# Optimization experiments

Measured on AMD Instinct MI355X. Metric: run time of the kernel, lower is better.

Reference implementation:

```python
import jax, jax.numpy as jnp
import numpy as np

B, Tin, Tout = 256, 32, 29
Venc, Vdec = 29, 72
E = 256; H = 256; L = 3; G = 4 * H; D = 2 * L  # bidirectional dirs * layers


def lstm_step(x, h, c, Wih0, Wih1, Whh, b):
    """One timestep of a 3-layer bidirectional LSTM (torch gate order i,f,g,o).
    x: [B, in], h/c: [D, B, H] in torch layout (layer-major, dir-minor)."""
    new_h, new_c = [], []
    inp = x
    for l in range(L):
        outs = []
        for d in range(2):
            idx = 2 * l + d
            Wih = Wih0[d] if l == 0 else Wih1[l - 1, d]
            g = inp @ Wih.T + h[idx] @ Whh[l, d].T + b[l, d]
            i_g, f_g, g_g, o_g = jnp.split(g, 4, axis=-1)
            cc = jax.nn.sigmoid(f_g) * c[idx] + jax.nn.sigmoid(i_g) * jnp.tanh(g_g)
            hh = jax.nn.sigmoid(o_g) * jnp.tanh(cc)
            new_h.append(hh); new_c.append(cc); outs.append(hh)
        inp = jnp.concatenate(outs, axis=-1)  # feeds next layer: [B, 2H]
    return jnp.stack(new_h), jnp.stack(new_c), inp


def proj(hid, W1, b1, W2, b2):
    """Linear over hidden dim then Linear over the layer*dir dim -- the exact
    math of torch's linear1 -> permute(2,1,0) -> linear2 -> permute(2,1,0)."""
    hn = jnp.einsum('lbh,gh->lbg', hid, W1) + b1            # [D, B, H]
    return jnp.einsum('lbh,ml->mbh', hn, W2) + b2[:, None, None]


def setup_inputs() -> dict:
    key = jax.random.key(0)
    ks = iter(jax.random.split(key, 64))
    def p(shape, scale=0.06):
        return jax.random.normal(next(ks), shape, jnp.float32) * scale
    return {
        "input": jax.random.randint(next(ks), (B, Tin), 0, Venc),
        "target": jax.random.randint(next(ks), (B, Tout), 0, Vdec),
        "teacher_force": 1,
        "enc_emb": p((Venc, E)), "dec_emb": p((Vdec, E)),
        "enc_Wih0": p((2, G, E)), "enc_Wih1": p((L - 1, 2, G, 2 * H)),
        "enc_Whh": p((L, 2, G, H)), "enc_b": p((L, 2, G)),
        "dec_Wih0": p((2, G, E)), "dec_Wih1": p((L - 1, 2, G, 2 * H)),
        "dec_Whh": p((L, 2, G, H)), "dec_b": p((L, 2, G)),
        "lin_h_W1": p((H, H)), "lin_h_b1": p((H,)), "lin_h_W2": p((D, D)), "lin_h_b2": p((D,)),
        "lin_c_W1": p((H, H)), "lin_c_b1": p((H,)), "lin_c_W2": p((D, D)), "lin_c_b2": p((D,)),
        "lin_a_W1": p((H, H)), "lin_a_b1": p((H,)), "lin_a_W2": p((D, D)), "lin_a_b2": p((D,)),
        "attn_W": p((E, E + H)), "attn_b": p((E,)),
        "fc_W": p((Vdec, 2 * H)), "fc_b": p((Vdec,)),
    }


def reference(input, target, teacher_force, enc_emb, dec_emb, enc_Wih0, enc_Wih1, enc_Whh, enc_b, dec_Wih0, dec_Wih1, dec_Whh, dec_b, lin_h_W1, lin_h_b1, lin_h_W2, lin_h_b2, lin_c_W1, lin_c_b1, lin_c_W2, lin_c_b2, lin_a_W1, lin_a_b1, lin_a_W2, lin_a_b2, attn_W, attn_b, fc_W, fc_b):
    Bb = input.shape[0]
    h0 = jnp.zeros((D, Bb, H), jnp.float32)

    # ---- encoder: step LSTM over Tin, projecting hidden per step for attention ----
    def enc_step(carry, x_t):
        h, c = carry
        h, c, _ = lstm_step(enc_emb[x_t], h, c, enc_Wih0, enc_Wih1, enc_Whh, enc_b)
        return (h, c), proj(h, lin_a_W1, lin_a_b1, lin_a_W2, lin_a_b2)

    (h, c), encoder_outputs = jax.lax.scan(enc_step, (h0, h0), input.T)  # [Tin, D, B, H]

    # ---- encoder->decoder state bridging (linear over H, linear over D) ----
    dec_h = proj(h, lin_h_W1, lin_h_b1, lin_h_W2, lin_h_b2)
    dec_c = proj(c, lin_c_W1, lin_c_b1, lin_c_W2, lin_c_b2)

    def dec_core(h, c, tok):
        emb = dec_emb[tok]                                # [B, E]
        energies = h[None] * encoder_outputs              # [Tin, D, B, H]
        aw = jax.nn.softmax(energies, axis=0)             # attn over source time
        ctx = (aw * encoder_outputs).sum(0).mean(0)       # [B, H]
        x = jnp.concatenate([emb, ctx], -1) @ attn_W.T + attn_b
        h, c, top = lstm_step(x, h, c, dec_Wih0, dec_Wih1, dec_Whh, dec_b)
        return h, c, top @ fc_W.T + fc_b, aw.sum(-1)      # logits [B,V], aw [Tin,D,B]

    if teacher_force:
        def step(carry, tok):
            h, c = carry
            h, c, logits, _ = dec_core(h, c, tok)
            return (h, c), logits
        _, logits_seq = jax.lax.scan(step, (dec_h, dec_c), target[:, :Tout - 1].T)
        attn_seq = jnp.zeros((Tout - 1, Tin, D, Bb), jnp.float32)
    else:
        def step(carry, _):
            h, c, tok = carry
            h, c, logits, aw = dec_core(h, c, tok)
            nxt = jnp.argmax(jax.nn.softmax(logits, -1), -1).astype(tok.dtype)
            return (h, c, nxt), (logits, aw)
        tok0 = jnp.ones((Bb,), input.dtype)
        _, (logits_seq, attn_seq) = jax.lax.scan(step, (dec_h, dec_c, tok0), None, length=Tout - 1)

    pred0 = jnp.zeros((1, Bb, Vdec), jnp.float32).at[0, :, 1].set(1.0)
    predicted = jnp.concatenate([pred0, logits_seq], 0)   # [Tout, B, Vdec]
    attn_weights = jnp.concatenate([jnp.zeros((1, Tin, D, Bb), jnp.float32), attn_seq], 0)
    return predicted, attn_weights
```

## Files before the change

kernel.cpp:

```cpp
#include <hip/hip_runtime.h>
#include <math.h>

#define BB 256
#define TIN 32
#define TOUT 29
#define VDEC 72
#define EDIM 256
#define HDIM 256
#define DD 6
#define BH (BB*HDIM)

typedef unsigned short u16;
typedef unsigned int u32;
typedef __bf16 bf16x8 __attribute__((ext_vector_type(8)));
typedef float f32x4 __attribute__((ext_vector_type(4)));
typedef u16 u16x8 __attribute__((ext_vector_type(8)));

__device__ __forceinline__ float sigmf(float x){ return 1.0f/(1.0f+expf(-x)); }
__device__ __forceinline__ u16 f2bf(float f){
  u32 u = __builtin_bit_cast(u32, f);
  u32 r = (u + 0x7fffu + ((u>>16)&1u)) >> 16;
  return (u16)r;
}
__device__ __forceinline__ float bf2f(u16 s){
  u32 u = ((u32)s)<<16; return __builtin_bit_cast(float, u);
}
__device__ __forceinline__ bf16x8 ldbf8(const u16* p){
  u16x8 t = *(const u16x8*)p; return __builtin_bit_cast(bf16x8, t);
}
__device__ __forceinline__ f32x4 mfma16(bf16x8 a, bf16x8 b, f32x4 c){
  return __builtin_amdgcn_mfma_f32_16x16x32_bf16(a, b, c, 0, 0, 0);
}

__global__ void fill_zero_u32(u32* __restrict__ p, int n){
  int i = blockIdx.x*256 + threadIdx.x;
  if (i < n) p[i] = 0u;
}

__global__ void init_out_kernel(float* __restrict__ out, int n){
  int i = blockIdx.x*256 + threadIdx.x;
  if (i >= n) return;
  float v = 0.0f;
  if (i < BB*VDEC && (i % VDEC) == 1) v = 1.0f;
  out[i] = v;
}

__global__ void bias2d_kernel(const float* __restrict__ W2a, const float* __restrict__ b1a, const float* __restrict__ b2a,
                              const float* __restrict__ W2h, const float* __restrict__ b1h, const float* __restrict__ b2h,
                              const float* __restrict__ W2c, const float* __restrict__ b1c, const float* __restrict__ b2c,
                              float* __restrict__ outp){
  int g = threadIdx.x;
  const float* W2[3] = {W2a, W2h, W2c};
  const float* b1[3] = {b1a, b1h, b1c};
  const float* b2[3] = {b2a, b2h, b2c};
  for (int p = 0; p < 3; p++)
    for (int m = 0; m < 6; m++){
      float s = 0.f;
      for (int l = 0; l < 6; l++) s += W2[p][m*6+l];
      outp[p*1536 + m*256 + g] = s * b1[p][g] + b2[p][m];
    }
}

__global__ void embed_enc_kernel(const int* __restrict__ input, const float* __restrict__ enc_emb,
                                 u16* __restrict__ x_emb){
  int i = blockIdx.x*256 + threadIdx.x;
  int e = i & 255, b = (i >> 8) & 255, t = i >> 16;
  x_emb[i] = f2bf(enc_emb[(size_t)input[b*TIN + t]*EDIM + e]);
}

__global__ void pack_w_kernel(const float* __restrict__ Wih, const float* __restrict__ Whh,
                              u16* __restrict__ dst, int K1, int K, int permute){
  int k = blockIdx.x*256 + threadIdx.x;
  int row = blockIdx.y;
  int d = row >> 10, rr = row & 1023;
  int g;
  if (permute){
    int ht = rr >> 6, r = rr & 63;
    g = (r>>4)*256 + ht*16 + (r&15);
  } else g = rr;
  float v;
  if (k < K1) v = Wih[((size_t)d*1024 + g)*K1 + k];
  else        v = Whh[((size_t)d*1024 + g)*256 + (k - K1)];
  dst[(size_t)row*K + k] = f2bf(v);
}

__global__ void mix_kernel(const float* __restrict__ inp, float* __restrict__ outp,
                           const float* __restrict__ W2, int n){
  int i = blockIdx.x*256 + threadIdx.x;
  if (i >= n) return;
  int h = i & 255, b = (i >> 8) & 255, t = i >> 16;
  size_t base = ((size_t)t*6)*BH + (size_t)b*256 + h;
  float v[6];
  #pragma unroll
  for (int l = 0; l < 6; l++) v[l] = inp[base + (size_t)l*BH];
  #pragma unroll
  for (int m = 0; m < 6; m++){
    float s = 0.f;
    #pragma unroll
    for (int l = 0; l < 6; l++) s += W2[m*6+l]*v[l];
    outp[base + (size_t)m*BH] = s;
  }
}

__global__ __launch_bounds__(256) void gemmN256_kernel(const float* __restrict__ A, float* __restrict__ C,
                                                       const float* __restrict__ W,
                                                       const float* __restrict__ bias2d,
                                                       u16* __restrict__ Cbf){
  __shared__ float As[32][33];
  __shared__ float Ws[256][34];
  int tid = threadIdx.x;
  int m_base = blockIdx.x * 32;
  int rg = tid >> 5, cg = tid & 31;
  float acc[4][8];
  #pragma unroll
  for (int i=0;i<4;i++)
    #pragma unroll
    for (int j=0;j<8;j++) acc[i][j]=0.f;
  for (int k0 = 0; k0 < 256; k0 += 32){
    #pragma unroll
    for (int p=0;p<4;p++) As[rg + p*8][cg] = A[(size_t)(m_base + rg + p*8)*256 + k0 + cg];
    #pragma unroll
    for (int p=0;p<32;p++) Ws[rg + p*8][cg] = W[(size_t)(rg + p*8)*256 + k0 + cg];
    __syncthreads();
    #pragma unroll
    for (int kk=0; kk<32; kk++){
      float a[4], w[8];
      #pragma unroll
      for (int i=0;i<4;i++) a[i] = As[rg*4+i][kk];
      #pragma unroll
      for (int j=0;j<8;j++) w[j] = Ws[cg*8+j][kk];
      #pragma unroll
      for (int i=0;i<4;i++)
        #pragma unroll
        for (int j=0;j<8;j++) acc[i][j] += a[i]*w[j];
    }
    __syncthreads();
  }
  #pragma unroll
  for (int i=0;i<4;i++){
    int row = m_base + rg*4 + i;
    int bm = (row >> 8) % 6;
    #pragma unroll
    for (int j=0;j<8;j++){
      float v = acc[i][j] + bias2d[bm*256 + cg*8 + j];
      C[(size_t)row*256 + cg*8 + j] = v;
      if (Cbf) Cbf[(size_t)row*256 + cg*8 + j] = f2bf(v);
    }
  }
}

__global__ __launch_bounds__(256) void lstm_stage_mfma(
    const u16* __restrict__ inp, int lda, int K1,
    const u16* __restrict__ Wpk,
    const float* __restrict__ bias_l,
    const u16* __restrict__ hR, u16* __restrict__ hW,
    float* __restrict__ cBuf, u16* __restrict__ inp_out,
    float* __restrict__ h_all_t, int l){
  __shared__ __align__(16) u16 As[32][72];
  __shared__ __align__(16) u16 Ws[64][72];
  __shared__ float Gt[4][32][17];
  int tid = threadIdx.x;
  int m_base = blockIdx.x*32;
  int d = blockIdx.y >> 4, ht = blockIdx.y & 15;
  int idx = 2*l + d;
  int K = K1 + 256;
  const u16* Wblk = Wpk + (size_t)((d*16+ht)*64)*K;
  const u16* A2 = hR + (size_t)idx*BH;
  int q = tid >> 6, lane = tid & 63;
  int ar = tid >> 3, kp = (tid & 7)*8;
  f32x4 acc0 = {0.f,0.f,0.f,0.f}, acc1 = {0.f,0.f,0.f,0.f};
  for (int c0 = 0; c0 < K; c0 += 64){
    int col = c0 + kp;
    const u16* ap = (col < K1) ? inp + (size_t)(m_base+ar)*lda + col
                               : A2  + (size_t)(m_base+ar)*HDIM + (col - K1);
    uint4 av  = *(const uint4*)ap;
    uint4 wv0 = *(const uint4*)(Wblk + (size_t)ar*K + col);
    uint4 wv1 = *(const uint4*)(Wblk + (size_t)(ar+32)*K + col);
    __syncthreads();
    *(uint4*)&As[ar][kp] = av;
    *(uint4*)&Ws[ar][kp] = wv0;
    *(uint4*)&Ws[ar+32][kp] = wv1;
    __syncthreads();
    #pragma unroll
    for (int kh = 0; kh < 2; kh++){
      int kb = kh*32 + (lane>>4)*8;
      bf16x8 a0 = ldbf8(&As[lane & 15][kb]);
      bf16x8 a1 = ldbf8(&As[16 + (lane & 15)][kb]);
      bf16x8 bq = ldbf8(&Ws[q*16 + (lane & 15)][kb]);
      acc0 = mfma16(a0, bq, acc0);
      acc1 = mfma16(a1, bq, acc1);
    }
  }
  int hh = lane & 15, rq = lane >> 4;
  #pragma unroll
  for (int r = 0; r < 4; r++){
    Gt[q][rq*4 + r][hh]      = acc0[r];
    Gt[q][16 + rq*4 + r][hh] = acc1[r];
  }
  __syncthreads();
  const float* bias = bias_l + d*1024;
  #pragma unroll
  for (int it = 0; it < 2; it++){
    int id = tid + it*256;
    int bb = id >> 4, h2 = id & 15;
    int b = m_base + bb, h = ht*16 + h2;
    float iv = Gt[0][bb][h2] + bias[h];
    float fv = Gt[1][bb][h2] + bias[256 + h];
    float gv = Gt[2][bb][h2] + bias[512 + h];
    float ov = Gt[3][bb][h2] + bias[768 + h];
    size_t off = (size_t)idx*BH + (size_t)b*HDIM + h;
    float cold = cBuf[off];
    float cc = sigmf(fv)*cold + sigmf(iv)*tanhf(gv);
    float hv = sigmf(ov)*tanhf(cc);
    cBuf[off] = cc;
    u16 hb = f2bf(hv);
    hW[off] = hb;
    inp_out[(size_t)b*512 + d*HDIM + h] = hb;
    if (h_all_t) h_all_t[off] = hv;
  }
}

__global__ __launch_bounds__(256) void xw_mfma(
    const u16* __restrict__ emb, const u16* __restrict__ ctx,
    const u16* __restrict__ Wpk, const float* __restrict__ bias,
    u16* __restrict__ xw){
  __shared__ __align__(16) u16 As[32][72];
  __shared__ __align__(16) u16 Ws[64][72];
  int tid = threadIdx.x;
  int m_base = blockIdx.x*32;
  int n_base = blockIdx.y*64;
  int q = tid >> 6, lane = tid & 63;
  int ar = tid >> 3, kp = (tid & 7)*8;
  const u16* Wblk = Wpk + (size_t)n_base*512;
  f32x4 acc0 = {0.f,0.f,0.f,0.f}, acc1 = {0.f,0.f,0.f,0.f};
  for (int c0 = 0; c0 < 512; c0 += 64){
    int col = c0 + kp;
    const u16* ap = (col < 256) ? emb + (size_t)(m_base+ar)*256 + col
                                : ctx + (size_t)(m_base+ar)*256 + (col - 256);
    uint4 av  = *(const uint4*)ap;
    uint4 wv0 = *(const uint4*)(Wblk + (size_t)ar*512 + col);
    uint4 wv1 = *(const uint4*)(Wblk + (size_t)(ar+32)*512 + col);
    __syncthreads();
    *(uint4*)&As[ar][kp] = av;
    *(uint4*)&Ws[ar][kp] = wv0;
    *(uint4*)&Ws[ar+32][kp] = wv1;
    __syncthreads();
    #pragma unroll
    for (int kh = 0; kh < 2; kh++){
      int kb = kh*32 + (lane>>4)*8;
      bf16x8 a0 = ldbf8(&As[lane & 15][kb]);
      bf16x8 a1 = ldbf8(&As[16 + (lane & 15)][kb]);
      bf16x8 bq = ldbf8(&Ws[q*16 + (lane & 15)][kb]);
      acc0 = mfma16(a0, bq, acc0);
      acc1 = mfma16(a1, bq, acc1);
    }
  }
  int hh = lane & 15, rq = lane >> 4;
  int n = n_base + q*16 + hh;
  float bv = bias[n];
  #pragma unroll
  for (int r = 0; r < 4; r++){
    xw[(size_t)(m_base + rq*4 + r)*256 + n]      = f2bf(acc0[r] + bv);
    xw[(size_t)(m_base + 16 + rq*4 + r)*256 + n] = f2bf(acc1[r] + bv);
  }
}

__global__ void attn_tok_kernel(const u16* __restrict__ hR, const float* __restrict__ eo,
                                u16* __restrict__ ctx, const int* __restrict__ tf,
                                float* __restrict__ attn_out, int step,
                                const int* __restrict__ target, const float* __restrict__ pred,
                                const float* __restrict__ dec_emb, u16* __restrict__ emb){
  int blk = blockIdx.x, tid = threadIdx.x;
  if (blk < 256){
    int i = blk*256 + tid;
    int hc = i & 255, b = i >> 8;
    bool wa = (tf[0] == 0);
    float acc = 0.f;
    for (int d = 0; d < DD; d++){
      float hv = bf2f(hR[(size_t)d*BH + (size_t)b*256 + hc]);
      const float* ep = eo + (size_t)d*BH + (size_t)b*256 + hc;
      float se = 0.f, ac = 0.f;
      for (int t = 0; t < TIN; t++){
        float ev = ep[(size_t)t*(DD*BH)];
        float e = expf(hv*ev);
        se += e; ac += e*ev;
      }
      acc += ac/se;
      if (wa){
        float inv = 1.f/se;
        for (int t = 0; t < TIN; t++){
          float ev = ep[(size_t)t*(DD*BH)];
          atomicAdd(&attn_out[(((size_t)(step+1)*TIN + t)*DD + d)*BB + b], expf(hv*ev)*inv);
        }
      }
    }
    ctx[i] = f2bf(acc*(1.0f/6.0f));
  } else {
    int j = (blk - 256)*256 + tid;
    int b = j >> 6, e4 = (j & 63)*4;
    int tok;
    if (tf[0]) tok = target[b*TOUT + step];
    else if (step == 0) tok = 1;
    else {
      const float* lg = pred + ((size_t)step*BB + b)*VDEC;
      tok = 0; float bv = lg[0];
      for (int v = 1; v < VDEC; v++){ float x = lg[v]; if (x > bv){ bv = x; tok = v; } }
    }
    #pragma unroll
    for (int r = 0; r < 4; r++)
      emb[(size_t)b*EDIM + e4 + r] = f2bf(dec_emb[(size_t)tok*EDIM + e4 + r]);
  }
}

__global__ void fc_kernel(const u16* __restrict__ top, const float* __restrict__ fc_W,
                          const float* __restrict__ fc_b, float* __restrict__ outp, int step){
  __shared__ float s[512];
  int b = blockIdx.x, tid = threadIdx.x;
  s[tid]       = bf2f(top[(size_t)b*512 + tid]);
  s[tid + 256] = bf2f(top[(size_t)b*512 + 256 + tid]);
  __syncthreads();
  if (tid < VDEC){
    float a = fc_b[tid];
    for (int k = 0; k < 512; k++) a += s[k]*fc_W[(size_t)tid*512 + k];
    outp[((size_t)(step+1)*BB + b)*VDEC + tid] = a;
  }
}


extern "C" void kernel_launch(void* const* d_in, const int* in_sizes, int n_in,
                              void* d_out, int out_size, void* d_ws, size_t ws_size,
                              hipStream_t stream){
  (void)in_sizes; (void)n_in; (void)out_size; (void)ws_size;
  const int*   input    = (const int*)d_in[0];
  const int*   target   = (const int*)d_in[1];
  const int*   tf       = (const int*)d_in[2];
  const float* enc_emb  = (const float*)d_in[3];
  const float* dec_emb  = (const float*)d_in[4];
  const float* enc_Wih0 = (const float*)d_in[5];
  const float* enc_Wih1 = (const float*)d_in[6];
  const float* enc_Whh  = (const float*)d_in[7];
  const float* enc_b    = (const float*)d_in[8];
  const float* dec_Wih0 = (const float*)d_in[9];
  const float* dec_Wih1 = (const float*)d_in[10];
  const float* dec_Whh  = (const float*)d_in[11];
  const float* dec_b    = (const float*)d_in[12];
  const float* lin_h_W1 = (const float*)d_in[13];
  const float* lin_h_b1 = (const float*)d_in[14];
  const float* lin_h_W2 = (const float*)d_in[15];
  const float* lin_h_b2 = (const float*)d_in[16];
  const float* lin_c_W1 = (const float*)d_in[17];
  const float* lin_c_b1 = (const float*)d_in[18];
  const float* lin_c_W2 = (const float*)d_in[19];
  const float* lin_c_b2 = (const float*)d_in[20];
  const float* lin_a_W1 = (const float*)d_in[21];
  const float* lin_a_b1 = (const float*)d_in[22];
  const float* lin_a_W2 = (const float*)d_in[23];
  const float* lin_a_b2 = (const float*)d_in[24];
  const float* attn_W   = (const float*)d_in[25];
  const float* attn_b   = (const float*)d_in[26];
  const float* fc_W     = (const float*)d_in[27];
  const float* fc_b     = (const float*)d_in[28];
  float* out = (float*)d_out;

  char* base = (char*)d_ws;
  size_t off = 0;
  auto alloc = [&](size_t bytes)->char*{
    char* p = base + off; off += (bytes + 255) & ~(size_t)255; return p;
  };
  float* h_all  = (float*)alloc(sizeof(float)*(size_t)TIN*DD*BH);
  float* tmp6   = (float*)alloc(sizeof(float)*(size_t)DD*BH);
  float* dec_c  = (float*)alloc(sizeof(float)*(size_t)DD*BH);
  float* bias2d = (float*)alloc(sizeof(float)*3*6*256);
  u16*   enc_hA = (u16*)alloc(sizeof(u16)*(size_t)DD*BH + sizeof(float)*(size_t)DD*BH);
  float* enc_c  = (float*)(enc_hA + (size_t)DD*BH);
  u16* enc_hB = (u16*)alloc(sizeof(u16)*(size_t)DD*BH);
  u16* dec_hA = (u16*)alloc(sizeof(u16)*(size_t)DD*BH);
  u16* dec_hB = (u16*)alloc(sizeof(u16)*(size_t)DD*BH);
  u16* x_emb  = (u16*)alloc(sizeof(u16)*(size_t)TIN*BB*EDIM);
  u16* bufA   = (u16*)alloc(sizeof(u16)*(size_t)BB*512);
  u16* bufB   = (u16*)alloc(sizeof(u16)*(size_t)BB*512);
  u16* emb    = (u16*)alloc(sizeof(u16)*(size_t)BB*256);
  u16* ctxb   = (u16*)alloc(sizeof(u16)*(size_t)BB*256);
  u16* xw     = (u16*)alloc(sizeof(u16)*(size_t)BB*256);
  u16* wp_e0  = (u16*)alloc(sizeof(u16)*(size_t)2048*512);
  u16* wp_e1  = (u16*)alloc(sizeof(u16)*(size_t)2048*768);
  u16* wp_e2  = (u16*)alloc(sizeof(u16)*(size_t)2048*768);
  u16* wp_d0  = (u16*)alloc(sizeof(u16)*(size_t)2048*512);
  u16* wp_d1  = (u16*)alloc(sizeof(u16)*(size_t)2048*768);
  u16* wp_d2  = (u16*)alloc(sizeof(u16)*(size_t)2048*768);
  u16* wp_at  = (u16*)alloc(sizeof(u16)*(size_t)256*512);

  const int outn = TOUT*BB*VDEC + TOUT*TIN*DD*BB;
  init_out_kernel<<<(outn+255)/256, 256, 0, stream>>>(out, outn);
  fill_zero_u32<<<(DD*BH*6/4 + 255)/256, 256, 0, stream>>>((u32*)enc_hA, DD*BH*6/4);
  bias2d_kernel<<<1, 256, 0, stream>>>(lin_a_W2, lin_a_b1, lin_a_b2,
                                       lin_h_W2, lin_h_b1, lin_h_b2,
                                       lin_c_W2, lin_c_b1, lin_c_b2, bias2d);
  embed_enc_kernel<<<(TIN*BB*EDIM)/256, 256, 0, stream>>>(input, enc_emb, x_emb);
  pack_w_kernel<<<dim3(2,2048), 256, 0, stream>>>(enc_Wih0, enc_Whh,                       wp_e0, 256, 512, 1);
  pack_w_kernel<<<dim3(3,2048), 256, 0, stream>>>(enc_Wih1, enc_Whh + 2*1024*256,          wp_e1, 512, 768, 1);
  pack_w_kernel<<<dim3(3,2048), 256, 0, stream>>>(enc_Wih1 + (size_t)2*1024*512, enc_Whh + 4*1024*256, wp_e2, 512, 768, 1);
  pack_w_kernel<<<dim3(2,2048), 256, 0, stream>>>(dec_Wih0, dec_Whh,                       wp_d0, 256, 512, 1);
  pack_w_kernel<<<dim3(3,2048), 256, 0, stream>>>(dec_Wih1, dec_Whh + 2*1024*256,          wp_d1, 512, 768, 1);
  pack_w_kernel<<<dim3(3,2048), 256, 0, stream>>>(dec_Wih1 + (size_t)2*1024*512, dec_Whh + 4*1024*256, wp_d2, 512, 768, 1);
  pack_w_kernel<<<dim3(2,256),  256, 0, stream>>>(attn_W, attn_W ,               wp_at, 512, 512, 0);

  dim3 sgrid(8, 32);
  for (int t = 0; t < TIN; t++){
    const u16* hRb = (t & 1) ? enc_hB : enc_hA;
    u16*       hWb = (t & 1) ? enc_hA : enc_hB;
    float* hat = h_all + (size_t)t*DD*BH;
    lstm_stage_mfma<<<sgrid,256,0,stream>>>(x_emb + (size_t)t*BB*EDIM, 256, 256, wp_e0,
        enc_b,        hRb, hWb, enc_c, bufA, hat, 0);
    lstm_stage_mfma<<<sgrid,256,0,stream>>>(bufA, 512, 512, wp_e1,
        enc_b + 2048, hRb, hWb, enc_c, bufB, hat, 1);
    lstm_stage_mfma<<<sgrid,256,0,stream>>>(bufB, 512, 512, wp_e2,
        enc_b + 4096, hRb, hWb, enc_c, bufA, hat, 2);
  }
  mix_kernel<<<BH/256, 256, 0, stream>>>(h_all + (size_t)31*DD*BH, tmp6, lin_h_W2, BH);
  gemmN256_kernel<<<(DD*BB)/32, 256, 0, stream>>>(tmp6, tmp6, lin_h_W1, bias2d + 1536, dec_hA);
  mix_kernel<<<BH/256, 256, 0, stream>>>(enc_c, tmp6, lin_c_W2, BH);
  gemmN256_kernel<<<(DD*BB)/32, 256, 0, stream>>>(tmp6, dec_c, lin_c_W1, bias2d + 3072, nullptr);
  mix_kernel<<<(TIN*BH)/256, 256, 0, stream>>>(h_all, h_all, lin_a_W2, TIN*BH);
  gemmN256_kernel<<<(TIN*DD*BB)/32, 256, 0, stream>>>(h_all, h_all, lin_a_W1, bias2d, nullptr);

  float* attn_out = out + (size_t)TOUT*BB*VDEC;
  for (int i = 0; i < TOUT-1; i++){
    const u16* hRb = (i & 1) ? dec_hB : dec_hA;
    u16*       hWb = (i & 1) ? dec_hA : dec_hB;
    attn_tok_kernel<<<320, 256, 0, stream>>>(hRb, h_all, ctxb, tf, attn_out, i,
                                             target, out, dec_emb, emb);
    xw_mfma<<<dim3(8,4), 256, 0, stream>>>(emb, ctxb, wp_at, attn_b, xw);
    lstm_stage_mfma<<<sgrid,256,0,stream>>>(xw, 256, 256, wp_d0,
        dec_b,        hRb, hWb, dec_c, bufA, nullptr, 0);
    lstm_stage_mfma<<<sgrid,256,0,stream>>>(bufA, 512, 512, wp_d1,
        dec_b + 2048, hRb, hWb, dec_c, bufB, nullptr, 1);
    lstm_stage_mfma<<<sgrid,256,0,stream>>>(bufB, 512, 512, wp_d2,
        dec_b + 4096, hRb, hWb, dec_c, bufA, nullptr, 2);
    fc_kernel<<<BB, 256, 0, stream>>>(bufA, fc_W, fc_b, out, i);
  }
}
```

Measured before the change: 3.463 ms.

## Fuse encoder/decoder loops into one persistent kernel with grid barriers

Replaces roughly two hundred per-step kernel launches with a single persistent mega-kernel of 256 blocks that synchronise through an atomic-counter grid barrier. It also folds the attention projection into the first decoder layer's weights, stores encoder outputs in bf16 with a batch-major layout, and moves the projection GEMMs to MFMA. The aim is to remove launch overhead and inter-kernel gaps on the serial recurrence. The trade-offs are that the spin barrier assumes all 256 blocks are co-resident, and bf16 storage of the attention keys adds rounding error.

```diff
diff --git a/kernel.cpp b/kernel.cpp
--- a/kernel.cpp
+++ b/kernel.cpp
@@ -9,6 +9,7 @@
 #define HDIM 256
 #define DD 6
 #define BH (BB*HDIM)
+#define NB 256
 
 typedef unsigned short u16;
 typedef unsigned int u32;
@@ -31,6 +32,7 @@
 __device__ __forceinline__ f32x4 mfma16(bf16x8 a, bf16x8 b, f32x4 c){
   return __builtin_amdgcn_mfma_f32_16x16x32_bf16(a, b, c, 0, 0, 0);
 }
+
 
 __global__ void fill_zero_u32(u32* __restrict__ p, int n){
   int i = blockIdx.x*256 + threadIdx.x;
@@ -69,102 +71,96 @@
 }
 
 __global__ void pack_w_kernel(const float* __restrict__ Wih, const float* __restrict__ Whh,
-                              u16* __restrict__ dst, int K1, int K, int permute){
+                              u16* __restrict__ dst, int K1, int K){
   int k = blockIdx.x*256 + threadIdx.x;
   int row = blockIdx.y;
   int d = row >> 10, rr = row & 1023;
-  int g;
-  if (permute){
-    int ht = rr >> 6, r = rr & 63;
-    g = (r>>4)*256 + ht*16 + (r&15);
-  } else g = rr;
+  int g = ((rr>>4)&3)*256 + (rr>>6)*16 + (rr&15);
   float v;
   if (k < K1) v = Wih[((size_t)d*1024 + g)*K1 + k];
   else        v = Whh[((size_t)d*1024 + g)*256 + (k - K1)];
   dst[(size_t)row*K + k] = f2bf(v);
 }
 
-__global__ void mix_kernel(const float* __restrict__ inp, float* __restrict__ outp,
-                           const float* __restrict__ W2, int n){
+__global__ void pack3_kernel(const float* __restrict__ a, const float* __restrict__ b, const float* __restrict__ c,
+                             u16* __restrict__ oa, u16* __restrict__ ob, u16* __restrict__ oc){
   int i = blockIdx.x*256 + threadIdx.x;
-  if (i >= n) return;
-  int h = i & 255, b = (i >> 8) & 255, t = i >> 16;
-  size_t base = ((size_t)t*6)*BH + (size_t)b*256 + h;
-  float v[6];
+  oa[i] = f2bf(a[i]); ob[i] = f2bf(b[i]); oc[i] = f2bf(c[i]);
+}
+
+__global__ __launch_bounds__(256) void comp_w_kernel(
+    const float* __restrict__ Wih0, const float* __restrict__ Whh0,
+    const float* __restrict__ attn_W, const float* __restrict__ attn_b,
+    const float* __restrict__ dec_b0, u16* __restrict__ wpk, float* __restrict__ b0p){
+  __shared__ float sw[8][256];
+  __shared__ float red[256];
+  int tid = threadIdx.x;
+  int rbase = blockIdx.x*8;
+  int gs[8], ds[8];
+  for (int r = 0; r < 8; r++){
+    int row = rbase + r;
+    int d = row >> 10, rr = row & 1023;
+    int g = ((rr>>4)&3)*256 + (rr>>6)*16 + (rr&15);
+    gs[r] = g; ds[r] = d;
+    sw[r][tid] = Wih0[((size_t)d*1024 + g)*256 + tid];
+  }
+  __syncthreads();
+  float a0[8], a1[8];
   #pragma unroll
-  for (int l = 0; l < 6; l++) v[l] = inp[base + (size_t)l*BH];
-  #pragma unroll
-  for (int m = 0; m < 6; m++){
-    float s = 0.f;
-    #pragma unroll
-    for (int l = 0; l < 6; l++) s += W2[m*6+l]*v[l];
-    outp[base + (size_t)m*BH] = s;
-  }
-}
-
-__global__ __launch_bounds__(256) void gemmN256_kernel(const float* __restrict__ A, float* __restrict__ C,
-                                                       const float* __restrict__ W,
-                                                       const float* __restrict__ bias2d,
-                                                       u16* __restrict__ Cbf){
-  __shared__ float As[32][33];
-  __shared__ float Ws[256][34];
-  int tid = threadIdx.x;
-  int m_base = blockIdx.x * 32;
-  int rg = tid >> 5, cg = tid & 31;
-  float acc[4][8];
-  #pragma unroll
-  for (int i=0;i<4;i++)
-    #pragma unroll
-    for (int j=0;j<8;j++) acc[i][j]=0.f;
-  for (int k0 = 0; k0 < 256; k0 += 32){
-    #pragma unroll
-    for (int p=0;p<4;p++) As[rg + p*8][cg] = A[(size_t)(m_base + rg + p*8)*256 + k0 + cg];
-    #pragma unroll
-    for (int p=0;p<32;p++) Ws[rg + p*8][cg] = W[(size_t)(rg + p*8)*256 + k0 + cg];
-    __syncthreads();
-    #pragma unroll
-    for (int kk=0; kk<32; kk++){
-      float a[4], w[8];
-      #pragma unroll
-      for (int i=0;i<4;i++) a[i] = As[rg*4+i][kk];
-      #pragma unroll
-      for (int j=0;j<8;j++) w[j] = Ws[cg*8+j][kk];
-      #pragma unroll
-      for (int i=0;i<4;i++)
-        #pragma unroll
-        for (int j=0;j<8;j++) acc[i][j] += a[i]*w[j];
-    }
-    __syncthreads();
-  }
-  #pragma unroll
-  for (int i=0;i<4;i++){
-    int row = m_base + rg*4 + i;
-    int bm = (row >> 8) % 6;
-    #pragma unroll
-    for (int j=0;j<8;j++){
-      float v = acc[i][j] + bias2d[bm*256 + cg*8 + j];
-      C[(size_t)row*256 + cg*8 + j] = v;
-      if (Cbf) Cbf[(size_t)row*256 + cg*8 + j] = f2bf(v);
-    }
-  }
-}
-
-__global__ __launch_bounds__(256) void lstm_stage_mfma(
+  for (int r = 0; r < 8; r++){ a0[r]=0.f; a1[r]=0.f; }
+  for (int e = 0; e < 256; e++){
+    float w0 = attn_W[(size_t)e*512 + tid];
+    float w1 = attn_W[(size_t)e*512 + 256 + tid];
+    #pragma unroll
+    for (int r = 0; r < 8; r++){ float s = sw[r][e]; a0[r] += s*w0; a1[r] += s*w1; }
+  }
+  for (int r = 0; r < 8; r++){
+    int row = rbase + r;
+    wpk[(size_t)row*768 + tid]       = f2bf(a0[r]);
+    wpk[(size_t)row*768 + 256 + tid] = f2bf(a1[r]);
+    wpk[(size_t)row*768 + 512 + tid] = f2bf(Whh0[((size_t)ds[r]*1024 + gs[r])*256 + tid]);
+  }
+  for (int r = 0; r < 8; r++){
+    red[tid] = sw[r][tid]*attn_b[tid];
+    __syncthreads();
+    for (int s2 = 128; s2 > 0; s2 >>= 1){ if (tid < s2) red[tid] += red[tid+s2]; __syncthreads(); }
+    if (tid == 0) b0p[ds[r]*1024 + gs[r]] = dec_b0[(size_t)ds[r]*1024 + gs[r]] + red[0];
+    __syncthreads();
+  }
+}
+
+
+__device__ __forceinline__ void gbar(int* cnt, int& ep){
+  __syncthreads();
+  ep++;
+  if (threadIdx.x == 0){
+    __threadfence();
+    __hip_atomic_fetch_add(cnt, 1, __ATOMIC_RELEASE, __HIP_MEMORY_SCOPE_AGENT);
+    int target = NB * ep;
+    while (__hip_atomic_load(cnt, __ATOMIC_ACQUIRE, __HIP_MEMORY_SCOPE_AGENT) < target)
+      __builtin_amdgcn_s_sleep(2);
+    __threadfence();
+  }
+  __syncthreads();
+}
+
+__device__ __forceinline__ void stage_unit(
     const u16* __restrict__ inp, int lda, int K1,
-    const u16* __restrict__ Wpk,
-    const float* __restrict__ bias_l,
+    const u16* __restrict__ Wpk, const float* __restrict__ bias_l,
     const u16* __restrict__ hR, u16* __restrict__ hW,
     float* __restrict__ cBuf, u16* __restrict__ inp_out,
-    float* __restrict__ h_all_t, int l){
-  __shared__ __align__(16) u16 As[32][72];
-  __shared__ __align__(16) u16 Ws[64][72];
-  __shared__ float Gt[4][32][17];
+    u16* __restrict__ h_all_t, int l, char* smem){
+  u16 (*As)[72] = (u16(*)[72])smem;
+  u16 (*Ws)[72] = (u16(*)[72])(smem + 4608);
+  float (*Gt)[32][17] = (float(*)[32][17])(smem + 13824);
   int tid = threadIdx.x;
-  int m_base = blockIdx.x*32;
-  int d = blockIdx.y >> 4, ht = blockIdx.y & 15;
+  int bid = blockIdx.x;
+  int m_base = (bid >> 5)*32;
+  int dht = bid & 31;
+  int d = dht >> 4, ht = dht & 15;
   int idx = 2*l + d;
   int K = K1 + 256;
-  const u16* Wblk = Wpk + (size_t)((d*16+ht)*64)*K;
+  const u16* Wblk = Wpk + (size_t)(dht*64)*K;
   const u16* A2 = hR + (size_t)idx*BH;
   int q = tid >> 6, lane = tid & 63;
   int ar = tid >> 3, kp = (tid & 7)*8;
@@ -184,11 +180,11 @@
     #pragma unroll
     for (int kh = 0; kh < 2; kh++){
       int kb = kh*32 + (lane>>4)*8;
-      bf16x8 a0 = ldbf8(&As[lane & 15][kb]);
-      bf16x8 a1 = ldbf8(&As[16 + (lane & 15)][kb]);
-      bf16x8 bq = ldbf8(&Ws[q*16 + (lane & 15)][kb]);
-      acc0 = mfma16(a0, bq, acc0);
-      acc1 = mfma16(a1, bq, acc1);
+      bf16x8 a0v = ldbf8(&As[lane & 15][kb]);
+      bf16x8 a1v = ldbf8(&As[16 + (lane & 15)][kb]);
+      bf16x8 bq  = ldbf8(&Ws[q*16 + (lane & 15)][kb]);
+      acc0 = mfma16(a0v, bq, acc0);
+      acc1 = mfma16(a1v, bq, acc1);
     }
   }
   int hh = lane & 15, rq = lane >> 4;
@@ -216,30 +212,25 @@
     u16 hb = f2bf(hv);
     hW[off] = hb;
     inp_out[(size_t)b*512 + d*HDIM + h] = hb;
-    if (h_all_t) h_all_t[off] = hv;
-  }
-}
-
-__global__ __launch_bounds__(256) void xw_mfma(
-    const u16* __restrict__ emb, const u16* __restrict__ ctx,
-    const u16* __restrict__ Wpk, const float* __restrict__ bias,
-    u16* __restrict__ xw){
-  __shared__ __align__(16) u16 As[32][72];
-  __shared__ __align__(16) u16 Ws[64][72];
+    if (h_all_t) h_all_t[off] = hb;
+  }
+}
+
+__device__ __forceinline__ void gemm_unit(
+    const u16* __restrict__ A, const u16* __restrict__ W,
+    const float* __restrict__ bias2, int r0, int n0, int mode,
+    u16* __restrict__ outb, float* __restrict__ outf, char* smem){
+  u16 (*As)[72] = (u16(*)[72])smem;
+  u16 (*Ws)[72] = (u16(*)[72])(smem + 4608);
   int tid = threadIdx.x;
-  int m_base = blockIdx.x*32;
-  int n_base = blockIdx.y*64;
   int q = tid >> 6, lane = tid & 63;
   int ar = tid >> 3, kp = (tid & 7)*8;
-  const u16* Wblk = Wpk + (size_t)n_base*512;
   f32x4 acc0 = {0.f,0.f,0.f,0.f}, acc1 = {0.f,0.f,0.f,0.f};
-  for (int c0 = 0; c0 < 512; c0 += 64){
+  for (int c0 = 0; c0 < 256; c0 += 64){
     int col = c0 + kp;
-    const u16* ap = (col < 256) ? emb + (size_t)(m_base+ar)*256 + col
-                                : ctx + (size_t)(m_base+ar)*256 + (col - 256);
-    uint4 av  = *(const uint4*)ap;
-    uint4 wv0 = *(const uint4*)(Wblk + (size_t)ar*512 + col);
-    uint4 wv1 = *(const uint4*)(Wblk + (size_t)(ar+32)*512 + col);
+    uint4 av  = *(const uint4*)(A + (size_t)(r0+ar)*256 + col);
+    uint4 wv0 = *(const uint4*)(W + (size_t)(n0+ar)*256 + col);
+    uint4 wv1 = *(const uint4*)(W + (size_t)(n0+ar+32)*256 + col);
     __syncthreads();
     *(uint4*)&As[ar][kp] = av;
     *(uint4*)&Ws[ar][kp] = wv0;
@@ -248,82 +239,202 @@
     #pragma unroll
     for (int kh = 0; kh < 2; kh++){
       int kb = kh*32 + (lane>>4)*8;
-      bf16x8 a0 = ldbf8(&As[lane & 15][kb]);
-      bf16x8 a1 = ldbf8(&As[16 + (lane & 15)][kb]);
-      bf16x8 bq = ldbf8(&Ws[q*16 + (lane & 15)][kb]);
-      acc0 = mfma16(a0, bq, acc0);
-      acc1 = mfma16(a1, bq, acc1);
+      bf16x8 a0v = ldbf8(&As[lane & 15][kb]);
+      bf16x8 a1v = ldbf8(&As[16 + (lane & 15)][kb]);
+      bf16x8 bq  = ldbf8(&Ws[q*16 + (lane & 15)][kb]);
+      acc0 = mfma16(a0v, bq, acc0);
+      acc1 = mfma16(a1v, bq, acc1);
     }
   }
   int hh = lane & 15, rq = lane >> 4;
-  int n = n_base + q*16 + hh;
-  float bv = bias[n];
+  int n = n0 + q*16 + hh;
   #pragma unroll
   for (int r = 0; r < 4; r++){
-    xw[(size_t)(m_base + rq*4 + r)*256 + n]      = f2bf(acc0[r] + bv);
-    xw[(size_t)(m_base + 16 + rq*4 + r)*256 + n] = f2bf(acc1[r] + bv);
-  }
-}
-
-__global__ void attn_tok_kernel(const u16* __restrict__ hR, const float* __restrict__ eo,
-                                u16* __restrict__ ctx, const int* __restrict__ tf,
-                                float* __restrict__ attn_out, int step,
-                                const int* __restrict__ target, const float* __restrict__ pred,
-                                const float* __restrict__ dec_emb, u16* __restrict__ emb){
-  int blk = blockIdx.x, tid = threadIdx.x;
-  if (blk < 256){
-    int i = blk*256 + tid;
-    int hc = i & 255, b = i >> 8;
-    bool wa = (tf[0] == 0);
-    float acc = 0.f;
-    for (int d = 0; d < DD; d++){
-      float hv = bf2f(hR[(size_t)d*BH + (size_t)b*256 + hc]);
-      const float* ep = eo + (size_t)d*BH + (size_t)b*256 + hc;
-      float se = 0.f, ac = 0.f;
+    #pragma unroll
+    for (int half = 0; half < 2; half++){
+      int row = r0 + half*16 + rq*4 + r;
+      float v = (half ? acc1[r] : acc0[r]) + bias2[((row>>8)%6)*256 + n];
+      if (mode == 0)      outb[(size_t)row*256 + n] = f2bf(v);
+      else if (mode == 1) outf[(size_t)row*256 + n] = v;
+      else {
+        int b = row & 255, mm = (row>>8)%6, t = row/1536;
+        outb[(((size_t)(b*6 + mm)*32 + t)*256) + n] = f2bf(v);
+      }
+    }
+  }
+}
+
+__device__ __forceinline__ void attn_unit(const u16* __restrict__ hR, const u16* __restrict__ eo2,
+                                          u16* __restrict__ embctx, const int* __restrict__ tf,
+                                          float* __restrict__ attn_out, int step, int b){
+  int hc = threadIdx.x;
+  bool wa = (tf[0] == 0);
+  float acc = 0.f;
+  for (int d = 0; d < 6; d++){
+    float hv = bf2f(hR[(size_t)d*BH + (size_t)b*256 + hc]);
+    const u16* base = eo2 + ((size_t)(b*6 + d)*32)*256 + hc;
+    float se = 0.f, ac = 0.f;
+    #pragma unroll 8
+    for (int t = 0; t < TIN; t++){
+      float ev = bf2f(base[t*256]);
+      float e = expf(hv*ev);
+      se += e; ac += e*ev;
+    }
+    acc += ac/se;
+    if (wa){
+      float inv = 1.f/se;
       for (int t = 0; t < TIN; t++){
-        float ev = ep[(size_t)t*(DD*BH)];
-        float e = expf(hv*ev);
-        se += e; ac += e*ev;
+        float ev = bf2f(base[t*256]);
+        atomicAdd(&attn_out[(((size_t)(step+1)*TIN + t)*DD + d)*BB + b], expf(hv*ev)*inv);
       }
-      acc += ac/se;
-      if (wa){
-        float inv = 1.f/se;
-        for (int t = 0; t < TIN; t++){
-          float ev = ep[(size_t)t*(DD*BH)];
-          atomicAdd(&attn_out[(((size_t)(step+1)*TIN + t)*DD + d)*BB + b], expf(hv*ev)*inv);
-        }
-      }
-    }
-    ctx[i] = f2bf(acc*(1.0f/6.0f));
-  } else {
-    int j = (blk - 256)*256 + tid;
-    int b = j >> 6, e4 = (j & 63)*4;
-    int tok;
-    if (tf[0]) tok = target[b*TOUT + step];
-    else if (step == 0) tok = 1;
-    else {
-      const float* lg = pred + ((size_t)step*BB + b)*VDEC;
-      tok = 0; float bv = lg[0];
-      for (int v = 1; v < VDEC; v++){ float x = lg[v]; if (x > bv){ bv = x; tok = v; } }
-    }
-    #pragma unroll
-    for (int r = 0; r < 4; r++)
-      emb[(size_t)b*EDIM + e4 + r] = f2bf(dec_emb[(size_t)tok*EDIM + e4 + r]);
-  }
-}
-
-__global__ void fc_kernel(const u16* __restrict__ top, const float* __restrict__ fc_W,
-                          const float* __restrict__ fc_b, float* __restrict__ outp, int step){
-  __shared__ float s[512];
-  int b = blockIdx.x, tid = threadIdx.x;
+    }
+  }
+  embctx[(size_t)b*512 + 256 + hc] = f2bf(acc*(1.0f/6.0f));
+}
+
+__device__ __forceinline__ void fc_unit(const u16* __restrict__ top, const float* __restrict__ fc_W,
+                                        const float* __restrict__ fc_b, float* __restrict__ out,
+                                        int slot, int b, char* smem){
+  float* s  = (float*)smem;
+  float* lg = (float*)(smem + 2048);
+  int tid = threadIdx.x;
   s[tid]       = bf2f(top[(size_t)b*512 + tid]);
   s[tid + 256] = bf2f(top[(size_t)b*512 + 256 + tid]);
   __syncthreads();
   if (tid < VDEC){
     float a = fc_b[tid];
     for (int k = 0; k < 512; k++) a += s[k]*fc_W[(size_t)tid*512 + k];
-    outp[((size_t)(step+1)*BB + b)*VDEC + tid] = a;
-  }
+    out[((size_t)slot*256 + b)*VDEC + tid] = a;
+    lg[tid] = a;
+  }
+  __syncthreads();
+}
+
+__device__ __forceinline__ void emb_unit(int i, const int* __restrict__ tf, const int* __restrict__ target,
+                                         const float* __restrict__ lg, const float* __restrict__ dec_emb,
+                                         u16* __restrict__ embctx, int b, char* smem){
+  int* tokp = (int*)(smem + 2368);
+  int tid = threadIdx.x;
+  if (tid == 0){
+    int tok;
+    if (tf[0]) tok = target[b*TOUT + i];
+    else if (i == 0) tok = 1;
+    else {
+      tok = 0; float bv = lg[0];
+      for (int v = 1; v < VDEC; v++){ float x = lg[v]; if (x > bv){ bv = x; tok = v; } }
+    }
+    *tokp = tok;
+  }
+  __syncthreads();
+  int tok = *tokp;
+  embctx[(size_t)b*512 + tid] = f2bf(dec_emb[(size_t)tok*EDIM + tid]);
+  __syncthreads();
+}
+
+struct MegaArgs {
+  const int *target, *tf;
+  const float *enc_b, *dec_b, *fc_W, *fc_b, *dec_emb;
+  const float *lin_h_W2, *lin_c_W2, *lin_a_W2;
+  const u16 *x_emb, *wp_e0, *wp_e1, *wp_e2, *wp_dc0, *wp_d1, *wp_d2;
+  const float *dc_b0p;
+  const u16 *w1h, *w1c, *w1a;
+  const float *bias2d;
+  u16 *h_all_bf, *enc_hA, *enc_hB;
+  float *enc_c;
+  u16 *tmp6hc;
+  u16 *eo2, *dec_hA, *dec_hB;
+  float *dec_c;
+  u16 *bufA, *bufB, *bufC, *embctx;
+  float *out, *attn_out;
+  int *cnt;
+};
+
+__global__ __launch_bounds__(256, 1) void mega_kernel(MegaArgs a){
+  __shared__ __align__(16) char smem[23040];
+  int ep = 0;
+  int bid = blockIdx.x, tid = threadIdx.x;
+  for (int t = 0; t < TIN; t++){
+    const u16* hR = (t & 1) ? a.enc_hB : a.enc_hA;
+    u16* hW = (t & 1) ? a.enc_hA : a.enc_hB;
+    u16* hat = a.h_all_bf + (size_t)t*6*BH;
+    stage_unit(a.x_emb + (size_t)t*BB*256, 256, 256, a.wp_e0, a.enc_b,        hR, hW, a.enc_c, a.bufA, hat, 0, smem);
+    gbar(a.cnt, ep);
+    stage_unit(a.bufA, 512, 512, a.wp_e1, a.enc_b + 2048, hR, hW, a.enc_c, a.bufB, hat, 1, smem);
+    gbar(a.cnt, ep);
+    stage_unit(a.bufB, 512, 512, a.wp_e2, a.enc_b + 4096, hR, hW, a.enc_c, a.bufA, hat, 2, smem);
+    gbar(a.cnt, ep);
+  }
+  {
+    float* sW2 = (float*)smem;
+    if (tid < 108){
+      int p = tid/36, j = tid%36;
+      const float* src = (p==0)? a.lin_h_W2 : (p==1 ? a.lin_c_W2 : a.lin_a_W2);
+      sW2[tid] = src[j];
+    }
+    __syncthreads();
+    int b = bid, h = tid;
+    float v[6];
+    #pragma unroll
+    for (int l2 = 0; l2 < 6; l2++) v[l2] = bf2f(a.h_all_bf[((size_t)(31*6 + l2)*BB + b)*256 + h]);
+    #pragma unroll
+    for (int m = 0; m < 6; m++){
+      float o = 0.f;
+      #pragma unroll
+      for (int l2 = 0; l2 < 6; l2++) o += sW2[m*6+l2]*v[l2];
+      a.tmp6hc[((size_t)(m*256 + b))*256 + h] = f2bf(o);
+    }
+    #pragma unroll
+    for (int l2 = 0; l2 < 6; l2++) v[l2] = a.enc_c[(size_t)l2*BH + (size_t)b*256 + h];
+    #pragma unroll
+    for (int m = 0; m < 6; m++){
+      float o = 0.f;
+      #pragma unroll
+      for (int l2 = 0; l2 < 6; l2++) o += sW2[36 + m*6+l2]*v[l2];
+      a.tmp6hc[((size_t)(1536 + m*256 + b))*256 + h] = f2bf(o);
+    }
+    for (int t = 0; t < TIN; t++){
+      #pragma unroll
+      for (int l2 = 0; l2 < 6; l2++) v[l2] = bf2f(a.h_all_bf[((size_t)(t*6 + l2)*BB + b)*256 + h]);
+      #pragma unroll
+      for (int m = 0; m < 6; m++){
+        float o = 0.f;
+        #pragma unroll
+        for (int l2 = 0; l2 < 6; l2++) o += sW2[72 + m*6+l2]*v[l2];
+        a.h_all_bf[((size_t)(t*6 + m)*BB + b)*256 + h] = f2bf(o);
+      }
+    }
+  }
+  gbar(a.cnt, ep);
+  for (int u = bid; u < 6528; u += NB){
+    if (u < 192){
+      int r0 = (u>>2)*32, n0 = (u&3)*64;
+      gemm_unit(a.tmp6hc, a.w1h, a.bias2d + 1536, r0, n0, 0, a.dec_hA, nullptr, smem);
+    } else if (u < 384){
+      int v2 = u - 192;
+      int r0 = (v2>>2)*32, n0 = (v2&3)*64;
+      gemm_unit(a.tmp6hc + (size_t)1536*256, a.w1c, a.bias2d + 3072, r0, n0, 1, nullptr, a.dec_c, smem);
+    } else {
+      int at = u - 384;
+      int r0 = (at>>2)*32, n0 = (at&3)*64;
+      gemm_unit(a.h_all_bf, a.w1a, a.bias2d, r0, n0, 2, a.eo2, nullptr, smem);
+    }
+  }
+  gbar(a.cnt, ep);
+  for (int i = 0; i < TOUT-1; i++){
+    const u16* hR = (i & 1) ? a.dec_hB : a.dec_hA;
+    u16* hW = (i & 1) ? a.dec_hA : a.dec_hB;
+    attn_unit(hR, a.eo2, a.embctx, a.tf, a.attn_out, i, bid);
+    if (i > 0) fc_unit(a.bufC, a.fc_W, a.fc_b, a.out, i, bid, smem);
+    emb_unit(i, a.tf, a.target, (const float*)(smem + 2048), a.dec_emb, a.embctx, bid, smem);
+    gbar(a.cnt, ep);
+    stage_unit(a.embctx, 512, 512, a.wp_dc0, a.dc_b0p,       hR, hW, a.dec_c, a.bufA, nullptr, 0, smem);
+    gbar(a.cnt, ep);
+    stage_unit(a.bufA, 512, 512, a.wp_d1, a.dec_b + 2048, hR, hW, a.dec_c, a.bufB, nullptr, 1, smem);
+    gbar(a.cnt, ep);
+    stage_unit(a.bufB, 512, 512, a.wp_d2, a.dec_b + 4096, hR, hW, a.dec_c, a.bufC, nullptr, 2, smem);
+    gbar(a.cnt, ep);
+  }
+  fc_unit(a.bufC, a.fc_W, a.fc_b, a.out, TOUT-1, bid, smem);
 }
 
 
@@ -367,76 +478,60 @@
   auto alloc = [&](size_t bytes)->char*{
     char* p = base + off; off += (bytes + 255) & ~(size_t)255; return p;
   };
-  float* h_all  = (float*)alloc(sizeof(float)*(size_t)TIN*DD*BH);
-  float* tmp6   = (float*)alloc(sizeof(float)*(size_t)DD*BH);
+  int*   cnt    = (int*)alloc(256);
+  u16*   enc_hA = (u16*)alloc(sizeof(u16)*(size_t)DD*BH);
+  float* enc_c  = (float*)alloc(sizeof(float)*(size_t)DD*BH);
+  size_t zero_u32 = (256 + sizeof(u16)*(size_t)DD*BH + sizeof(float)*(size_t)DD*BH)/4;
+
+  u16*   enc_hB = (u16*)alloc(sizeof(u16)*(size_t)DD*BH);
+  u16*   dec_hA = (u16*)alloc(sizeof(u16)*(size_t)DD*BH);
+  u16*   dec_hB = (u16*)alloc(sizeof(u16)*(size_t)DD*BH);
   float* dec_c  = (float*)alloc(sizeof(float)*(size_t)DD*BH);
+  u16*   tmp6hc = (u16*)alloc(sizeof(u16)*(size_t)2*1536*256);
+  u16*   h_all  = (u16*)alloc(sizeof(u16)*(size_t)TIN*DD*BH);
+  u16*   eo2    = (u16*)alloc(sizeof(u16)*(size_t)TIN*DD*BH);
+  u16*   x_emb  = (u16*)alloc(sizeof(u16)*(size_t)TIN*BB*EDIM);
+  u16*   bufA   = (u16*)alloc(sizeof(u16)*(size_t)BB*512);
+  u16*   bufB   = (u16*)alloc(sizeof(u16)*(size_t)BB*512);
+  u16*   bufC   = (u16*)alloc(sizeof(u16)*(size_t)BB*512);
+  u16*   embctx = (u16*)alloc(sizeof(u16)*(size_t)BB*512);
   float* bias2d = (float*)alloc(sizeof(float)*3*6*256);
-  u16*   enc_hA = (u16*)alloc(sizeof(u16)*(size_t)DD*BH + sizeof(float)*(size_t)DD*BH);
-  float* enc_c  = (float*)(enc_hA + (size_t)DD*BH);
-  u16* enc_hB = (u16*)alloc(sizeof(u16)*(size_t)DD*BH);
-  u16* dec_hA = (u16*)alloc(sizeof(u16)*(size_t)DD*BH);
-  u16* dec_hB = (u16*)alloc(sizeof(u16)*(size_t)DD*BH);
-  u16* x_emb  = (u16*)alloc(sizeof(u16)*(size_t)TIN*BB*EDIM);
-  u16* bufA   = (u16*)alloc(sizeof(u16)*(size_t)BB*512);
-  u16* bufB   = (u16*)alloc(sizeof(u16)*(size_t)BB*512);
-  u16* emb    = (u16*)alloc(sizeof(u16)*(size_t)BB*256);
-  u16* ctxb   = (u16*)alloc(sizeof(u16)*(size_t)BB*256);
-  u16* xw     = (u16*)alloc(sizeof(u16)*(size_t)BB*256);
-  u16* wp_e0  = (u16*)alloc(sizeof(u16)*(size_t)2048*512);
-  u16* wp_e1  = (u16*)alloc(sizeof(u16)*(size_t)2048*768);
-  u16* wp_e2  = (u16*)alloc(sizeof(u16)*(size_t)2048*768);
-  u16* wp_d0  = (u16*)alloc(sizeof(u16)*(size_t)2048*512);
-  u16* wp_d1  = (u16*)alloc(sizeof(u16)*(size_t)2048*768);
-  u16* wp_d2  = (u16*)alloc(sizeof(u16)*(size_t)2048*768);
-  u16* wp_at  = (u16*)alloc(sizeof(u16)*(size_t)256*512);
+  float* dc_b0p = (float*)alloc(sizeof(float)*2048);
+  u16*   w1h    = (u16*)alloc(sizeof(u16)*65536);
+  u16*   w1c    = (u16*)alloc(sizeof(u16)*65536);
+  u16*   w1a    = (u16*)alloc(sizeof(u16)*65536);
+  u16*   wp_e0  = (u16*)alloc(sizeof(u16)*(size_t)2048*512);
+  u16*   wp_e1  = (u16*)alloc(sizeof(u16)*(size_t)2048*768);
+  u16*   wp_e2  = (u16*)alloc(sizeof(u16)*(size_t)2048*768);
+  u16*   wp_dc0 = (u16*)alloc(sizeof(u16)*(size_t)2048*768);
+  u16*   wp_d1  = (u16*)alloc(sizeof(u16)*(size_t)2048*768);
+  u16*   wp_d2  = (u16*)alloc(sizeof(u16)*(size_t)2048*768);
 
   const int outn = TOUT*BB*VDEC + TOUT*TIN*DD*BB;
   init_out_kernel<<<(outn+255)/256, 256, 0, stream>>>(out, outn);
-  fill_zero_u32<<<(DD*BH*6/4 + 255)/256, 256, 0, stream>>>((u32*)enc_hA, DD*BH*6/4);
+  fill_zero_u32<<<((int)zero_u32+255)/256, 256, 0, stream>>>((u32*)cnt, (int)zero_u32);
   bias2d_kernel<<<1, 256, 0, stream>>>(lin_a_W2, lin_a_b1, lin_a_b2,
                                        lin_h_W2, lin_h_b1, lin_h_b2,
                                        lin_c_W2, lin_c_b1, lin_c_b2, bias2d);
   embed_enc_kernel<<<(TIN*BB*EDIM)/256, 256, 0, stream>>>(input, enc_emb, x_emb);
-  pack_w_kernel<<<dim3(2,2048), 256, 0, stream>>>(enc_Wih0, enc_Whh,                       wp_e0, 256, 512, 1);
-  pack_w_kernel<<<dim3(3,2048), 256, 0, stream>>>(enc_Wih1, enc_Whh + 2*1024*256,          wp_e1, 512, 768, 1);
-  pack_w_kernel<<<dim3(3,2048), 256, 0, stream>>>(enc_Wih1 + (size_t)2*1024*512, enc_Whh + 4*1024*256, wp_e2, 512, 768, 1);
-  pack_w_kernel<<<dim3(2,2048), 256, 0, stream>>>(dec_Wih0, dec_Whh,                       wp_d0, 256, 512, 1);
-  pack_w_kernel<<<dim3(3,2048), 256, 0, stream>>>(dec_Wih1, dec_Whh + 2*1024*256,          wp_d1, 512, 768, 1);
-  pack_w_kernel<<<dim3(3,2048), 256, 0, stream>>>(dec_Wih1 + (size_t)2*1024*512, dec_Whh + 4*1024*256, wp_d2, 512, 768, 1);
-  pack_w_kernel<<<dim3(2,256),  256, 0, stream>>>(attn_W, attn_W ,               wp_at, 512, 512, 0);
-
-  dim3 sgrid(8, 32);
-  for (int t = 0; t < TIN; t++){
-    const u16* hRb = (t & 1) ? enc_hB : enc_hA;
-    u16*       hWb = (t & 1) ? enc_hA : enc_hB;
-    float* hat = h_all + (size_t)t*DD*BH;
-    lstm_stage_mfma<<<sgrid,256,0,stream>>>(x_emb + (size_t)t*BB*EDIM, 256, 256, wp_e0,
-        enc_b,        hRb, hWb, enc_c, bufA, hat, 0);
-    lstm_stage_mfma<<<sgrid,256,0,stream>>>(bufA, 512, 512, wp_e1,
-        enc_b + 2048, hRb, hWb, enc_c, bufB, hat, 1);
-    lstm_stage_mfma<<<sgrid,256,0,stream>>>(bufB, 512, 512, wp_e2,
-        enc_b + 4096, hRb, hWb, enc_c, bufA, hat, 2);
-  }
-  mix_kernel<<<BH/256, 256, 0, stream>>>(h_all + (size_t)31*DD*BH, tmp6, lin_h_W2, BH);
-  gemmN256_kernel<<<(DD*BB)/32, 256, 0, stream>>>(tmp6, tmp6, lin_h_W1, bias2d + 1536, dec_hA);
-  mix_kernel<<<BH/256, 256, 0, stream>>>(enc_c, tmp6, lin_c_W2, BH);
-  gemmN256_kernel<<<(DD*BB)/32, 256, 0, stream>>>(tmp6, dec_c, lin_c_W1, bias2d + 3072, nullptr);
-  mix_kernel<<<(TIN*BH)/256, 256, 0, stream>>>(h_all, h_all, lin_a_W2, TIN*BH);
-  gemmN256_kernel<<<(TIN*DD*BB)/32, 256, 0, stream>>>(h_all, h_all, lin_a_W1, bias2d, nullptr);
-
-  float* attn_out = out + (size_t)TOUT*BB*VDEC;
-  for (int i = 0; i < TOUT-1; i++){
-    const u16* hRb = (i & 1) ? dec_hB : dec_hA;
-    u16*       hWb = (i & 1) ? dec_hA : dec_hB;
-    attn_tok_kernel<<<320, 256, 0, stream>>>(hRb, h_all, ctxb, tf, attn_out, i,
-                                             target, out, dec_emb, emb);
-    xw_mfma<<<dim3(8,4), 256, 0, stream>>>(emb, ctxb, wp_at, attn_b, xw);
-    lstm_stage_mfma<<<sgrid,256,0,stream>>>(xw, 256, 256, wp_d0,
-        dec_b,        hRb, hWb, dec_c, bufA, nullptr, 0);
-    lstm_stage_mfma<<<sgrid,256,0,stream>>>(bufA, 512, 512, wp_d1,
-        dec_b + 2048, hRb, hWb, dec_c, bufB, nullptr, 1);
-    lstm_stage_mfma<<<sgrid,256,0,stream>>>(bufB, 512, 512, wp_d2,
-        dec_b + 4096, hRb, hWb, dec_c, bufA, nullptr, 2);
-    fc_kernel<<<BB, 256, 0, stream>>>(bufA, fc_W, fc_b, out, i);
-  }
-}
+  pack_w_kernel<<<dim3(2,2048), 256, 0, stream>>>(enc_Wih0, enc_Whh,                       wp_e0, 256, 512);
+  pack_w_kernel<<<dim3(3,2048), 256, 0, stream>>>(enc_Wih1, enc_Whh + 2*1024*256,          wp_e1, 512, 768);
+  pack_w_kernel<<<dim3(3,2048), 256, 0, stream>>>(enc_Wih1 + (size_t)2*1024*512, enc_Whh + 4*1024*256, wp_e2, 512, 768);
+  pack_w_kernel<<<dim3(3,2048), 256, 0, stream>>>(dec_Wih1, dec_Whh + 2*1024*256,          wp_d1, 512, 768);
+  pack_w_kernel<<<dim3(3,2048), 256, 0, stream>>>(dec_Wih1 + (size_t)2*1024*512, dec_Whh + 4*1024*256, wp_d2, 512, 768);
+  pack3_kernel<<<256, 256, 0, stream>>>(lin_h_W1, lin_c_W1, lin_a_W1, w1h, w1c, w1a);
+  comp_w_kernel<<<256, 256, 0, stream>>>(dec_Wih0, dec_Whh, attn_W, attn_b, dec_b, wp_dc0, dc_b0p);
+
+  MegaArgs a;
+  a.target = target; a.tf = tf;
+  a.enc_b = enc_b; a.dec_b = dec_b; a.fc_W = fc_W; a.fc_b = fc_b; a.dec_emb = dec_emb;
+  a.lin_h_W2 = lin_h_W2; a.lin_c_W2 = lin_c_W2; a.lin_a_W2 = lin_a_W2;
+  a.x_emb = x_emb; a.wp_e0 = wp_e0; a.wp_e1 = wp_e1; a.wp_e2 = wp_e2;
+  a.wp_dc0 = wp_dc0; a.wp_d1 = wp_d1; a.wp_d2 = wp_d2;
+  a.dc_b0p = dc_b0p; a.w1h = w1h; a.w1c = w1c; a.w1a = w1a; a.bias2d = bias2d;
+  a.h_all_bf = h_all; a.enc_hA = enc_hA; a.enc_hB = enc_hB; a.enc_c = enc_c;
+  a.tmp6hc = tmp6hc; a.eo2 = eo2; a.dec_hA = dec_hA; a.dec_hB = dec_hB; a.dec_c = dec_c;
+  a.bufA = bufA; a.bufB = bufB; a.bufC = bufC; a.embctx = embctx;
+  a.out = out; a.attn_out = out + (size_t)TOUT*BB*VDEC; a.cnt = cnt;
+  mega_kernel<<<NB, 256, 0, stream>>>(a);
+}
```

After: 7.351 ms. +112.3%, slower.
